# Performance work log

Measured on AMD Instinct MI355X. Metric: run time of the kernel, lower is better.

The kernel has to match this reference:

```python
import jax, jax.numpy as jnp
import numpy as np

N_BINS = 15  # matches _ECELoss(n_bins=15); boundaries are linspace(0,1,n_bins+1)
NUM_CLASSES = 128
N_SAMPLES = 1_000_000


def setup_inputs() -> dict:
    key = jax.random.key(0)
    k1, k2 = jax.random.split(key)
    logits = jax.random.normal(k1, (N_SAMPLES, NUM_CLASSES), dtype=jnp.float32) * 2.0
    labels = jax.random.randint(k2, (N_SAMPLES,), 0, NUM_CLASSES, dtype=jnp.int64)
    return {"logits": logits, "labels": labels}


def reference(logits, labels):
    # softmax + max/argmax (single pass)
    probs = jax.nn.softmax(logits, axis=1)
    confidences = jnp.max(probs, axis=1)            # [N]
    predictions = jnp.argmax(probs, axis=1)         # [N]
    accuracies = (predictions == labels).astype(jnp.float32)

    n = confidences.shape[0]
    # bin membership: conf > lower and conf <= upper with equal-width bins ->
    # bin index = ceil(conf * n_bins) - 1 (softmax conf > 0 so never exactly 0)
    bin_idx = jnp.clip(jnp.ceil(confidences * N_BINS).astype(jnp.int32) - 1, 0, N_BINS - 1)

    # single-pass histogram reductions: counts, sum(conf), sum(acc) per bin
    counts = jax.ops.segment_sum(jnp.ones_like(confidences), bin_idx, num_segments=N_BINS)
    conf_sum = jax.ops.segment_sum(confidences, bin_idx, num_segments=N_BINS)
    acc_sum = jax.ops.segment_sum(accuracies, bin_idx, num_segments=N_BINS)

    nonempty = counts > 0
    safe_counts = jnp.where(nonempty, counts, 1.0)
    gap = jnp.abs(conf_sum / safe_counts - acc_sum / safe_counts)
    # weighted by prop_in_bin = counts / n; empty bins contribute 0
    ece = jnp.sum(jnp.where(nonempty, gap * counts / n, 0.0))
    return ece.reshape(1)
```

## Files before the change

kernel.cpp:

```cpp
#include <hip/hip_runtime.h>
#include <math.h>

#define N_BINS 15
#define NUM_CLASSES 128
#define LOG2E 1.4426950408889634f

template <int CTRL>
__device__ __forceinline__ float dpp_f(float x) {
    return __int_as_float(__builtin_amdgcn_update_dpp(
        0, __float_as_int(x), CTRL, 0xF, 0xF, true));
}
template <int CTRL>
__device__ __forceinline__ int dpp_i(int x) {
    return __builtin_amdgcn_update_dpp(0, x, CTRL, 0xF, 0xF, true);
}

__device__ __forceinline__ float rowmax16(float m) {
    m = fmaxf(m, dpp_f<0xB1>(m));
    m = fmaxf(m, dpp_f<0x4E>(m));
    m = fmaxf(m, dpp_f<0x141>(m));
    m = fmaxf(m, dpp_f<0x140>(m));
    return m;
}
__device__ __forceinline__ float rowsum16(float x) {
    x += dpp_f<0xB1>(x);
    x += dpp_f<0x4E>(x);
    x += dpp_f<0x141>(x);
    x += dpp_f<0x140>(x);
    return x;
}
__device__ __forceinline__ int rowmin16(int x) {
    x = min(x, dpp_i<0xB1>(x));
    x = min(x, dpp_i<0x4E>(x));
    x = min(x, dpp_i<0x141>(x));
    x = min(x, dpp_i<0x140>(x));
    return x;
}

__device__ __forceinline__ void process_row(
    float4 ca, float4 cb, int colbase, bool leader, int lab, bool valid,
    float* s_conf, float* s_acc, unsigned int* s_cnt)
{
    const float t0 = fmaxf(fmaxf(ca.x, ca.y), ca.z);
    const float t1 = fmaxf(fmaxf(ca.w, cb.x), cb.y);
    const float t2 = fmaxf(fmaxf(cb.z, cb.w), t0);
    float m = fmaxf(t1, t2);
    m = rowmax16(m);

    const float nmL = -m * LOG2E;
    float e0 = __builtin_amdgcn_exp2f(fmaf(ca.x, LOG2E, nmL));
    float e1 = __builtin_amdgcn_exp2f(fmaf(ca.y, LOG2E, nmL));
    float e2 = __builtin_amdgcn_exp2f(fmaf(ca.z, LOG2E, nmL));
    float e3 = __builtin_amdgcn_exp2f(fmaf(ca.w, LOG2E, nmL));
    float e4 = __builtin_amdgcn_exp2f(fmaf(cb.x, LOG2E, nmL));
    float e5 = __builtin_amdgcn_exp2f(fmaf(cb.y, LOG2E, nmL));
    float e6 = __builtin_amdgcn_exp2f(fmaf(cb.z, LOG2E, nmL));
    float e7 = __builtin_amdgcn_exp2f(fmaf(cb.w, LOG2E, nmL));
    float e = ((e0 + e1) + (e2 + e3)) + ((e4 + e5) + (e6 + e7));
    e = rowsum16(e);

    const int INF = 0x7FFFFFFF;
    const int c0 = (ca.x == m) ? colbase      : INF;
    const int c1 = (ca.y == m) ? colbase + 1  : INF;
    const int c2 = (ca.z == m) ? colbase + 2  : INF;
    const int c3 = (ca.w == m) ? colbase + 3  : INF;
    const int c4 = (cb.x == m) ? colbase + 64 : INF;
    const int c5 = (cb.y == m) ? colbase + 65 : INF;
    const int c6 = (cb.z == m) ? colbase + 66 : INF;
    const int c7 = (cb.w == m) ? colbase + 67 : INF;
    const int m1 = min(min(c0, c1), c2);
    const int m2 = min(min(c3, c4), c5);
    const int m3 = min(min(c6, c7), m1);
    int idx = min(m2, m3);
    idx = rowmin16(idx);

    if (valid && leader) {
        const float conf = __builtin_amdgcn_rcpf(e);
        int bin = (int)ceilf(conf * (float)N_BINS) - 1;
        bin = min(max(bin, 0), N_BINS - 1);
        atomicAdd(&s_conf[bin], conf);
        atomicAdd(&s_acc[bin], (idx == lab) ? 1.0f : 0.0f);
        atomicAdd(&s_cnt[bin], 1u);
    }
}

__global__ __launch_bounds__(256) void ece_pass1(
    const float* __restrict__ logits,
    const int* __restrict__ labels,
    int n,
    double* __restrict__ conf_sum,
    double* __restrict__ acc_sum,
    unsigned int* __restrict__ counts)
{
    __shared__ float s_conf[N_BINS];
    __shared__ float s_acc[N_BINS];
    __shared__ unsigned int s_cnt[N_BINS];

    const int t = threadIdx.x;
    if (t < N_BINS) { s_conf[t] = 0.f; s_acc[t] = 0.f; s_cnt[t] = 0u; }
    __syncthreads();

    const int lane = t & 63;
    const int g    = lane >> 4;
    const int s    = lane & 15;
    const bool leader = (s == 0);
    const int colbase = 4 * s;

    const int wid = (blockIdx.x << 2) | (t >> 6);
    const int nw  = gridDim.x << 2;
    const unsigned rstep = (unsigned)nw * 8u;
    const unsigned bstep = rstep * 512u;

    int nfull = 0;
    {
        const int lim = n - 8 - wid * 8;
        if (lim >= 0) nfull = lim / (int)rstep + 1;
    }

    const char* __restrict__ Lg = (const char*)logits;
    const unsigned row0 = (unsigned)(wid * 8 + g);
    unsigned off  = row0 * 512u + (unsigned)s * 16u;
    unsigned lrow = row0;

    float4 a0, a1, b0, b1;
    if (nfull > 0) {
        a0 = *(const float4*)(Lg + off);
        a1 = *(const float4*)(Lg + off + 256u);
        b0 = *(const float4*)(Lg + off + 2048u);
        b1 = *(const float4*)(Lg + off + 2304u);
    }

    for (int k = 0; k < nfull; ++k) {
        const int labA = labels[lrow];
        const int labB = labels[lrow + 4u];
        const float4 ca0 = a0, ca1 = a1, cb0 = b0, cb1 = b1;

        const unsigned noff = off + bstep;
        if (k + 1 < nfull) {
            a0 = *(const float4*)(Lg + noff);
            a1 = *(const float4*)(Lg + noff + 256u);
            b0 = *(const float4*)(Lg + noff + 2048u);
            b1 = *(const float4*)(Lg + noff + 2304u);
        }

        process_row(ca0, ca1, colbase, leader, labA, true, s_conf, s_acc, s_cnt);
        process_row(cb0, cb1, colbase, leader, labB, true, s_conf, s_acc, s_cnt);

        off = noff;
        lrow += rstep;
    }

    {
        const unsigned tbase = (unsigned)(wid * 8) + (unsigned)nfull * rstep;
        if (tbase < (unsigned)n) {
            const unsigned rA = tbase + (unsigned)g;
            const unsigned rB = rA + 4u;
            const bool vA = rA < (unsigned)n;
            const bool vB = rB < (unsigned)n;
            const unsigned cA = vA ? rA : (unsigned)(n - 1);
            const unsigned cB = vB ? rB : (unsigned)(n - 1);
            const unsigned oA = cA * 512u + (unsigned)s * 16u;
            const unsigned oB = cB * 512u + (unsigned)s * 16u;
            float4 ta0 = *(const float4*)(Lg + oA);
            float4 ta1 = *(const float4*)(Lg + oA + 256u);
            float4 tb0 = *(const float4*)(Lg + oB);
            float4 tb1 = *(const float4*)(Lg + oB + 256u);
            const int labA = vA ? labels[rA] : -1;
            const int labB = vB ? labels[rB] : -1;
            process_row(ta0, ta1, colbase, leader, labA, vA, s_conf, s_acc, s_cnt);
            process_row(tb0, tb1, colbase, leader, labB, vB, s_conf, s_acc, s_cnt);
        }
    }

    __syncthreads();
    if (t < N_BINS && s_cnt[t] != 0u) {
        atomicAdd(&conf_sum[t], (double)s_conf[t]);
        atomicAdd(&acc_sum[t], (double)s_acc[t]);
        atomicAdd(&counts[t], s_cnt[t]);
    }
}

__global__ void ece_pass2(const double* __restrict__ conf_sum,
                          const double* __restrict__ acc_sum,
                          const unsigned int* __restrict__ counts,
                          int n, float* __restrict__ out)
{
    double ece = 0.0;
    #pragma unroll
    for (int b = 0; b < N_BINS; ++b) {
        const unsigned int c = counts[b];
        if (c != 0u) {
            const double cd = (double)c;
            const double gap = fabs(conf_sum[b] / cd - acc_sum[b] / cd);
            ece += gap * cd / (double)n;
        }
    }
    out[0] = (float)ece;
}

extern "C" void kernel_launch(void* const* d_in, const int* in_sizes, int n_in,
                              void* d_out, int out_size, void* d_ws, size_t ws_size,
                              hipStream_t stream)
{
    const float* logits = (const float*)d_in[0];
    const int*   labels = (const int*)d_in[1];
    const int n = in_sizes[1];

    double* conf_sum = (double*)d_ws;
    double* acc_sum  = conf_sum + N_BINS;
    unsigned int* counts = (unsigned int*)(acc_sum + N_BINS);

    hipMemsetAsync(d_ws, 0, N_BINS * (sizeof(double) * 2 + sizeof(unsigned int)),
                   stream);

    const int blocks = 2048;
    ece_pass1<<<blocks, 256, 0, stream>>>(logits, labels, n,
                                          conf_sum, acc_sum, counts);
    ece_pass2<<<1, 1, 0, stream>>>(conf_sum, acc_sum, counts, n, (float*)d_out);
}
```

Measured before the change: 127.0 us.

## Fuse ECE finalize into main kernel via last-block ticket and deepen prefetch

Removes the separate finalize kernel: each block takes an atomic ticket after flushing its bins, and the last block reads the global sums and computes the ECE. It also drops the per-bin count histogram, since gap*count/n reduces to |conf_sum-acc_sum|/n. The loop now double-buffers two iterations of loads, labels included, to keep more memory requests in flight, and launch bounds request 8 waves per SIMD. In exchange it adds a threadfence, a global atomic and an extra sync per block, and uses s_conf!=0 as the non-empty test.

```diff
diff --git a/kernel.cpp b/kernel.cpp
--- a/kernel.cpp
+++ b/kernel.cpp
@@ -2,7 +2,6 @@
 #include <math.h>
 
 #define N_BINS 15
-#define NUM_CLASSES 128
 #define LOG2E 1.4426950408889634f
 
 template <int CTRL>
@@ -39,7 +38,7 @@
 
 __device__ __forceinline__ void process_row(
     float4 ca, float4 cb, int colbase, bool leader, int lab, bool valid,
-    float* s_conf, float* s_acc, unsigned int* s_cnt)
+    float* s_conf, float* s_acc)
 {
     const float t0 = fmaxf(fmaxf(ca.x, ca.y), ca.z);
     const float t1 = fmaxf(fmaxf(ca.w, cb.x), cb.y);
@@ -80,24 +79,34 @@
         bin = min(max(bin, 0), N_BINS - 1);
         atomicAdd(&s_conf[bin], conf);
         atomicAdd(&s_acc[bin], (idx == lab) ? 1.0f : 0.0f);
-        atomicAdd(&s_cnt[bin], 1u);
-    }
-}
-
-__global__ __launch_bounds__(256) void ece_pass1(
+    }
+}
+
+__device__ __forceinline__ void load_iter(const char* __restrict__ Lg,
+    unsigned off, float4& t0, float4& t1, float4& t2, float4& t3)
+{
+    t0 = *(const float4*)(Lg + off);
+    t1 = *(const float4*)(Lg + off + 256u);
+    t2 = *(const float4*)(Lg + off + 2048u);
+    t3 = *(const float4*)(Lg + off + 2304u);
+}
+
+__global__ __launch_bounds__(256, 8) void ece_fused(
     const float* __restrict__ logits,
     const int* __restrict__ labels,
     int n,
     double* __restrict__ conf_sum,
     double* __restrict__ acc_sum,
-    unsigned int* __restrict__ counts)
+    unsigned int* __restrict__ ticket,
+    float* __restrict__ out)
 {
     __shared__ float s_conf[N_BINS];
     __shared__ float s_acc[N_BINS];
-    __shared__ unsigned int s_cnt[N_BINS];
+    __shared__ double s_term[N_BINS];
+    __shared__ bool s_last;
 
     const int t = threadIdx.x;
-    if (t < N_BINS) { s_conf[t] = 0.f; s_acc[t] = 0.f; s_cnt[t] = 0u; }
+    if (t < N_BINS) { s_conf[t] = 0.f; s_acc[t] = 0.f; }
     __syncthreads();
 
     const int lane = t & 63;
@@ -119,35 +128,43 @@
 
     const char* __restrict__ Lg = (const char*)logits;
     const unsigned row0 = (unsigned)(wid * 8 + g);
-    unsigned off  = row0 * 512u + (unsigned)s * 16u;
-    unsigned lrow = row0;
-
-    float4 a0, a1, b0, b1;
-    if (nfull > 0) {
-        a0 = *(const float4*)(Lg + off);
-        a1 = *(const float4*)(Lg + off + 256u);
-        b0 = *(const float4*)(Lg + off + 2048u);
-        b1 = *(const float4*)(Lg + off + 2304u);
-    }
-
-    for (int k = 0; k < nfull; ++k) {
-        const int labA = labels[lrow];
-        const int labB = labels[lrow + 4u];
-        const float4 ca0 = a0, ca1 = a1, cb0 = b0, cb1 = b1;
-
-        const unsigned noff = off + bstep;
-        if (k + 1 < nfull) {
-            a0 = *(const float4*)(Lg + noff);
-            a1 = *(const float4*)(Lg + noff + 256u);
-            b0 = *(const float4*)(Lg + noff + 2048u);
-            b1 = *(const float4*)(Lg + noff + 2304u);
-        }
-
-        process_row(ca0, ca1, colbase, leader, labA, true, s_conf, s_acc, s_cnt);
-        process_row(cb0, cb1, colbase, leader, labB, true, s_conf, s_acc, s_cnt);
-
-        off = noff;
-        lrow += rstep;
+
+    unsigned offX = row0 * 512u + (unsigned)s * 16u;
+    unsigned offY = offX + bstep;
+    unsigned lrX = row0;
+    unsigned lrY = row0 + rstep;
+    float4 x0, x1, x2, x3, y0, y1, y2, y3;
+    int labAx = -1, labBx = -1, labAy = -1, labBy = -1;
+
+    if (nfull >= 1) {
+        load_iter(Lg, offX, x0, x1, x2, x3);
+        labAx = labels[lrX]; labBx = labels[lrX + 4u];
+    }
+    if (nfull >= 2) {
+        load_iter(Lg, offY, y0, y1, y2, y3);
+        labAy = labels[lrY]; labBy = labels[lrY + 4u];
+    }
+
+    int k = 0;
+    for (; k + 1 < nfull; k += 2) {
+        process_row(x0, x1, colbase, leader, labAx, true, s_conf, s_acc);
+        process_row(x2, x3, colbase, leader, labBx, true, s_conf, s_acc);
+        if (k + 2 < nfull) {
+            offX += 2u * bstep; lrX += 2u * rstep;
+            load_iter(Lg, offX, x0, x1, x2, x3);
+            labAx = labels[lrX]; labBx = labels[lrX + 4u];
+        }
+        process_row(y0, y1, colbase, leader, labAy, true, s_conf, s_acc);
+        process_row(y2, y3, colbase, leader, labBy, true, s_conf, s_acc);
+        if (k + 3 < nfull) {
+            offY += 2u * bstep; lrY += 2u * rstep;
+            load_iter(Lg, offY, y0, y1, y2, y3);
+            labAy = labels[lrY]; labBy = labels[lrY + 4u];
+        }
+    }
+    if (k < nfull) {
+        process_row(x0, x1, colbase, leader, labAx, true, s_conf, s_acc);
+        process_row(x2, x3, colbase, leader, labBx, true, s_conf, s_acc);
     }
 
     {
@@ -167,35 +184,39 @@
             float4 tb1 = *(const float4*)(Lg + oB + 256u);
             const int labA = vA ? labels[rA] : -1;
             const int labB = vB ? labels[rB] : -1;
-            process_row(ta0, ta1, colbase, leader, labA, vA, s_conf, s_acc, s_cnt);
-            process_row(tb0, tb1, colbase, leader, labB, vB, s_conf, s_acc, s_cnt);
-        }
-    }
-
-    __syncthreads();
-    if (t < N_BINS && s_cnt[t] != 0u) {
+            process_row(ta0, ta1, colbase, leader, labA, vA, s_conf, s_acc);
+            process_row(tb0, tb1, colbase, leader, labB, vB, s_conf, s_acc);
+        }
+    }
+
+    __syncthreads();
+    if (t < N_BINS && s_conf[t] != 0.f) {
         atomicAdd(&conf_sum[t], (double)s_conf[t]);
         atomicAdd(&acc_sum[t], (double)s_acc[t]);
-        atomicAdd(&counts[t], s_cnt[t]);
-    }
-}
-
-__global__ void ece_pass2(const double* __restrict__ conf_sum,
-                          const double* __restrict__ acc_sum,
-                          const unsigned int* __restrict__ counts,
-                          int n, float* __restrict__ out)
-{
-    double ece = 0.0;
-    #pragma unroll
-    for (int b = 0; b < N_BINS; ++b) {
-        const unsigned int c = counts[b];
-        if (c != 0u) {
-            const double cd = (double)c;
-            const double gap = fabs(conf_sum[b] / cd - acc_sum[b] / cd);
-            ece += gap * cd / (double)n;
-        }
-    }
-    out[0] = (float)ece;
+    }
+    __syncthreads();
+
+    if (t == 0) {
+        __threadfence();
+        const unsigned prev = atomicAdd(ticket, 1u);
+        s_last = (prev == (unsigned)(gridDim.x - 1));
+    }
+    __syncthreads();
+
+    if (s_last) {
+        if (t < N_BINS) {
+            const double cs = atomicAdd(&conf_sum[t], 0.0);
+            const double as = atomicAdd(&acc_sum[t], 0.0);
+            s_term[t] = fabs(cs - as) / (double)n;
+        }
+        __syncthreads();
+        if (t == 0) {
+            double ece = 0.0;
+            #pragma unroll
+            for (int b = 0; b < N_BINS; ++b) ece += s_term[b];
+            out[0] = (float)ece;
+        }
+    }
 }
 
 extern "C" void kernel_launch(void* const* d_in, const int* in_sizes, int n_in,
@@ -208,13 +229,13 @@
 
     double* conf_sum = (double*)d_ws;
     double* acc_sum  = conf_sum + N_BINS;
-    unsigned int* counts = (unsigned int*)(acc_sum + N_BINS);
-
-    hipMemsetAsync(d_ws, 0, N_BINS * (sizeof(double) * 2 + sizeof(unsigned int)),
+    unsigned int* ticket = (unsigned int*)(acc_sum + N_BINS);
+
+    hipMemsetAsync(d_ws, 0, N_BINS * sizeof(double) * 2 + sizeof(unsigned int),
                    stream);
 
     const int blocks = 2048;
-    ece_pass1<<<blocks, 256, 0, stream>>>(logits, labels, n,
-                                          conf_sum, acc_sum, counts);
-    ece_pass2<<<1, 1, 0, stream>>>(conf_sum, acc_sum, counts, n, (float*)d_out);
-}
+    ece_fused<<<blocks, 256, 0, stream>>>(logits, labels, n,
+                                          conf_sum, acc_sum, ticket,
+                                          (float*)d_out);
+}
```

Result: slower. 187.7 us (+47.7%).

## Drop bin counts algebraically and fuse finalize into main kernel via ticket

Applied to the files above, without the earlier changes.

Rewrites the per-bin term gap*count/n as |conf_sum-acc_sum|/n, which removes the count histogram and its shared and global atomics. Replaces the separate single-thread finalize kernel with a last-block-done ticket inside the main kernel. This aims to cut one kernel launch and per-row LDS atomics. It adds a threadfence and a global ticket atomic per block, and it depends on the memset zeroing the ticket each call.

```diff
diff --git a/kernel.cpp b/kernel.cpp
--- a/kernel.cpp
+++ b/kernel.cpp
@@ -2,7 +2,6 @@
 #include <math.h>
 
 #define N_BINS 15
-#define NUM_CLASSES 128
 #define LOG2E 1.4426950408889634f
 
 template <int CTRL>
@@ -39,7 +38,7 @@
 
 __device__ __forceinline__ void process_row(
     float4 ca, float4 cb, int colbase, bool leader, int lab, bool valid,
-    float* s_conf, float* s_acc, unsigned int* s_cnt)
+    float* s_conf, float* s_acc)
 {
     const float t0 = fmaxf(fmaxf(ca.x, ca.y), ca.z);
     const float t1 = fmaxf(fmaxf(ca.w, cb.x), cb.y);
@@ -80,24 +79,25 @@
         bin = min(max(bin, 0), N_BINS - 1);
         atomicAdd(&s_conf[bin], conf);
         atomicAdd(&s_acc[bin], (idx == lab) ? 1.0f : 0.0f);
-        atomicAdd(&s_cnt[bin], 1u);
-    }
-}
-
-__global__ __launch_bounds__(256) void ece_pass1(
+    }
+}
+
+__global__ __launch_bounds__(256) void ece_fused(
     const float* __restrict__ logits,
     const int* __restrict__ labels,
     int n,
     double* __restrict__ conf_sum,
     double* __restrict__ acc_sum,
-    unsigned int* __restrict__ counts)
+    unsigned int* __restrict__ ticket,
+    float* __restrict__ out)
 {
     __shared__ float s_conf[N_BINS];
     __shared__ float s_acc[N_BINS];
-    __shared__ unsigned int s_cnt[N_BINS];
+    __shared__ double s_term[N_BINS];
+    __shared__ bool s_last;
 
     const int t = threadIdx.x;
-    if (t < N_BINS) { s_conf[t] = 0.f; s_acc[t] = 0.f; s_cnt[t] = 0u; }
+    if (t < N_BINS) { s_conf[t] = 0.f; s_acc[t] = 0.f; }
     __syncthreads();
 
     const int lane = t & 63;
@@ -143,8 +143,8 @@
             b1 = *(const float4*)(Lg + noff + 2304u);
         }
 
-        process_row(ca0, ca1, colbase, leader, labA, true, s_conf, s_acc, s_cnt);
-        process_row(cb0, cb1, colbase, leader, labB, true, s_conf, s_acc, s_cnt);
+        process_row(ca0, ca1, colbase, leader, labA, true, s_conf, s_acc);
+        process_row(cb0, cb1, colbase, leader, labB, true, s_conf, s_acc);
 
         off = noff;
         lrow += rstep;
@@ -167,35 +167,39 @@
             float4 tb1 = *(const float4*)(Lg + oB + 256u);
             const int labA = vA ? labels[rA] : -1;
             const int labB = vB ? labels[rB] : -1;
-            process_row(ta0, ta1, colbase, leader, labA, vA, s_conf, s_acc, s_cnt);
-            process_row(tb0, tb1, colbase, leader, labB, vB, s_conf, s_acc, s_cnt);
-        }
-    }
-
-    __syncthreads();
-    if (t < N_BINS && s_cnt[t] != 0u) {
+            process_row(ta0, ta1, colbase, leader, labA, vA, s_conf, s_acc);
+            process_row(tb0, tb1, colbase, leader, labB, vB, s_conf, s_acc);
+        }
+    }
+
+    __syncthreads();
+    if (t < N_BINS && s_conf[t] != 0.f) {
         atomicAdd(&conf_sum[t], (double)s_conf[t]);
         atomicAdd(&acc_sum[t], (double)s_acc[t]);
-        atomicAdd(&counts[t], s_cnt[t]);
-    }
-}
-
-__global__ void ece_pass2(const double* __restrict__ conf_sum,
-                          const double* __restrict__ acc_sum,
-                          const unsigned int* __restrict__ counts,
-                          int n, float* __restrict__ out)
-{
-    double ece = 0.0;
-    #pragma unroll
-    for (int b = 0; b < N_BINS; ++b) {
-        const unsigned int c = counts[b];
-        if (c != 0u) {
-            const double cd = (double)c;
-            const double gap = fabs(conf_sum[b] / cd - acc_sum[b] / cd);
-            ece += gap * cd / (double)n;
-        }
-    }
-    out[0] = (float)ece;
+    }
+    __syncthreads();
+
+    if (t == 0) {
+        __threadfence();
+        const unsigned prev = atomicAdd(ticket, 1u);
+        s_last = (prev == (unsigned)(gridDim.x - 1));
+    }
+    __syncthreads();
+
+    if (s_last) {
+        if (t < N_BINS) {
+            const double cs = atomicAdd(&conf_sum[t], 0.0);
+            const double as = atomicAdd(&acc_sum[t], 0.0);
+            s_term[t] = fabs(cs - as) / (double)n;
+        }
+        __syncthreads();
+        if (t == 0) {
+            double ece = 0.0;
+            #pragma unroll
+            for (int b = 0; b < N_BINS; ++b) ece += s_term[b];
+            out[0] = (float)ece;
+        }
+    }
 }
 
 extern "C" void kernel_launch(void* const* d_in, const int* in_sizes, int n_in,
@@ -208,13 +212,13 @@
 
     double* conf_sum = (double*)d_ws;
     double* acc_sum  = conf_sum + N_BINS;
-    unsigned int* counts = (unsigned int*)(acc_sum + N_BINS);
-
-    hipMemsetAsync(d_ws, 0, N_BINS * (sizeof(double) * 2 + sizeof(unsigned int)),
+    unsigned int* ticket = (unsigned int*)(acc_sum + N_BINS);
+
+    hipMemsetAsync(d_ws, 0, N_BINS * sizeof(double) * 2 + sizeof(unsigned int),
                    stream);
 
     const int blocks = 2048;
-    ece_pass1<<<blocks, 256, 0, stream>>>(logits, labels, n,
-                                          conf_sum, acc_sum, counts);
-    ece_pass2<<<1, 1, 0, stream>>>(conf_sum, acc_sum, counts, n, (float*)d_out);
-}
+    ece_fused<<<blocks, 256, 0, stream>>>(logits, labels, n,
+                                          conf_sum, acc_sum, ticket,
+                                          (float*)d_out);
+}
```

New measurement: 188.4 us. 1.48x slower.
